# Kernel tuning notes

Hardware: AMD Instinct MI355X
Metric: run time of the kernel (lower is better)

## Reference

```python
import jax, jax.numpy as jnp
import numpy as np

B, S, D = 4, 4096, 1024
H, HID, ATT = 16, 64, 64


def setup_inputs() -> dict:
    key = jax.random.key(0)
    ks = jax.random.split(key, 7)
    sc = 0.02
    return {
        "x": jax.random.normal(ks[0], (B, S, D), dtype=jnp.float32),
        "Wq": jax.random.normal(ks[1], (D, H * HID), dtype=jnp.float32) * sc,
        "bq": jnp.zeros((H * HID,), dtype=jnp.float32),
        "Wk": jax.random.normal(ks[2], (D, H * HID), dtype=jnp.float32) * sc,
        "bk": jnp.zeros((H * HID,), dtype=jnp.float32),
        "Wv": jax.random.normal(ks[3], (D, H * ATT), dtype=jnp.float32) * sc,
        "bv": jnp.zeros((H * ATT,), dtype=jnp.float32),
    }


def reference(x, Wq, bq, Wk, bk, Wv, bv):
    b, s, _ = x.shape
    q = (x @ Wq + bq).reshape(b, s, H, HID)
    k = (x @ Wk + bk).reshape(b, s, H, HID)
    v = (x @ Wv + bv).reshape(b, s, H, ATT)
    # attention across the head axis: [B,S,H,H] scores per token
    scores = jnp.einsum("bsid,bsjd->bsij", q, k) / np.sqrt(HID).astype(np.float32)
    probs = jax.nn.softmax(scores, axis=-1)
    ctx = jnp.einsum("bsij,bsja->bsia", probs, v)
    return ctx.reshape(b, s, H * ATT)
```

## Files before the change

kernel.cpp:

```cpp
#include <hip/hip_runtime.h>


#define AS1 __attribute__((address_space(1)))
#define AS3 __attribute__((address_space(3)))

typedef __bf16 bf16x8 __attribute__((ext_vector_type(8)));
typedef float f32x4 __attribute__((ext_vector_type(4)));
typedef unsigned short u16x8 __attribute__((ext_vector_type(8)));

static constexpr int MTOK = 16384;
static constexpr int N3   = 3072;
static constexpr int KD   = 1024;

__device__ __forceinline__ unsigned short f2bf(float f) {
  unsigned u = __float_as_uint(f);
  unsigned r = u + 0x7FFFu + ((u >> 16) & 1u);
  return (unsigned short)(r >> 16);
}
__device__ __forceinline__ float bf2f(unsigned short s) {
  return __uint_as_float(((unsigned)s) << 16);
}

__device__ __forceinline__ void gload_lds16(const void* g, void* lds_uniform) {
  __builtin_amdgcn_global_load_lds((const AS1 void*)g, (AS3 void*)lds_uniform, 16, 0, 0);
}

__global__ __launch_bounds__(256) void cvt_x_kernel(const float* __restrict__ x,
                                                    unsigned short* __restrict__ xb) {
  int i = blockIdx.x * 256 + threadIdx.x;
  const float4* p = (const float4*)x;
  float4 a = p[2 * i], b = p[2 * i + 1];
  u16x8 o;
  o[0] = f2bf(a.x); o[1] = f2bf(a.y); o[2] = f2bf(a.z); o[3] = f2bf(a.w);
  o[4] = f2bf(b.x); o[5] = f2bf(b.y); o[6] = f2bf(b.z); o[7] = f2bf(b.w);
  *((u16x8*)xb + i) = o;
}

__global__ __launch_bounds__(256) void prep_w_kernel(const float* __restrict__ Wq,
                                                     const float* __restrict__ Wk,
                                                     const float* __restrict__ Wv,
                                                     const float* __restrict__ bq,
                                                     const float* __restrict__ bk,
                                                     const float* __restrict__ bv,
                                                     unsigned short* __restrict__ WT,
                                                     float* __restrict__ bcat) {
  __shared__ float tile[32][33];
  int kt = blockIdx.x * 32;
  int nt = blockIdx.y * 32;
  const float* W; const float* bias; int nb;
  if (nt < 1024)      { W = Wq; bias = bq; nb = nt; }
  else if (nt < 2048) { W = Wk; bias = bk; nb = nt - 1024; }
  else                { W = Wv; bias = bv; nb = nt - 2048; }
  int tx = threadIdx.x & 31, ty = threadIdx.x >> 5;
#pragma unroll
  for (int it = 0; it < 4; ++it) {
    int kk = it * 8 + ty;
    tile[kk][tx] = W[(size_t)(kt + kk) * 1024 + nb + tx];
  }
  __syncthreads();
#pragma unroll
  for (int it = 0; it < 4; ++it) {
    int nn = it * 8 + ty;
    WT[(size_t)(nt + nn) * 1024 + kt + tx] = f2bf(tile[tx][nn]);
  }
  if (blockIdx.x == 0 && threadIdx.x < 32)
    bcat[nt + threadIdx.x] = bias[nb + threadIdx.x];
}

__global__ __launch_bounds__(512, 2) void gemm_qkv_kernel(const unsigned short* __restrict__ A,
                                                          const unsigned short* __restrict__ Bt,
                                                          const float* __restrict__ bias,
                                                          unsigned short* __restrict__ C) {
  __shared__ __align__(16) unsigned short lds[65536];
  const int tid  = threadIdx.x;
  const int lane = tid & 63;
  const int wave = tid >> 6;
  const int wm = wave >> 2, wn = wave & 3;
  const int m0 = blockIdx.x * 256;
  const int n0 = blockIdx.y * 256;
  const int chunk = lane >> 4;
  const int hl = lane & 15;

  const int srow = tid >> 2;
  const int sc   = ((tid & 3) ^ ((srow >> 1) & 3)) * 8;
  const size_t asrc0 = (size_t)(m0 + srow) * KD + sc;
  const size_t asrc1 = (size_t)(m0 + 128 + srow) * KD + sc;
  const size_t bsrc0 = (size_t)(n0 + srow) * KD + sc;
  const size_t bsrc1 = (size_t)(n0 + 128 + srow) * KD + sc;

  int aoff[8], boff[4];
#pragma unroll
  for (int m = 0; m < 8; ++m) {
    int row = wm * 128 + m * 16 + hl;
    aoff[m] = row * 32 + (chunk ^ ((row >> 1) & 3)) * 8;
  }
#pragma unroll
  for (int n = 0; n < 4; ++n) {
    int row = wn * 64 + n * 16 + hl;
    boff[n] = 8192 + row * 32 + (chunk ^ ((row >> 1) & 3)) * 8;
  }

  f32x4 acc[8][4] = {};

#define STAGE(SLOT, KK)                                                        \
  do {                                                                         \
    unsigned short* dst = lds + (SLOT) * 16384 + tid * 8;                      \
    gload_lds16(A  + asrc0 + (KK), dst);                                       \
    gload_lds16(A  + asrc1 + (KK), dst + 4096);                                \
    gload_lds16(Bt + bsrc0 + (KK), dst + 8192);                                \
    gload_lds16(Bt + bsrc1 + (KK), dst + 12288);                               \
  } while (0)

#define PH(SLOT, DOSTAGE, STSLOT, KREAD)                                       \
  do {                                                                         \
    const unsigned short* bufp = lds + (SLOT) * 16384;                         \
    bf16x8 af[8], bfr[4];                                                      \
    _Pragma("unroll") for (int m = 0; m < 8; ++m)                              \
      af[m] = *(const bf16x8*)(bufp + aoff[m]);                                \
    _Pragma("unroll") for (int n = 0; n < 4; ++n)                              \
      bfr[n] = *(const bf16x8*)(bufp + boff[n]);                               \
    if (DOSTAGE) { STAGE(STSLOT, (KREAD) + 96); }                              \
    __builtin_amdgcn_s_barrier();                             \
    asm volatile("s_waitcnt lgkmcnt(0)" ::: "memory");                         \
    __builtin_amdgcn_sched_barrier(0);                                         \
    __builtin_amdgcn_s_setprio(1);                                             \
    _Pragma("unroll") for (int m = 0; m < 8; ++m)                              \
      _Pragma("unroll") for (int n = 0; n < 4; ++n)                            \
        acc[m][n] = __builtin_amdgcn_mfma_f32_16x16x32_bf16(af[m], bfr[n],     \
                                                            acc[m][n], 0, 0, 0);\
    __builtin_amdgcn_s_setprio(0);                                             \
  } while (0)

#define SYNC(VM)                                                               \
  do {                                                                         \
    asm volatile("s_waitcnt vmcnt(" #VM ")" ::: "memory");                     \
    __builtin_amdgcn_s_barrier();                             \
    __builtin_amdgcn_sched_barrier(0);                                         \
  } while (0)

  STAGE(0, 0); STAGE(1, 32); STAGE(2, 64);

#pragma unroll 1
  for (int t = 0; t < 7; ++t) {
    const int kb = t * 128;
    SYNC(8); PH(0, true, 3, kb);
    SYNC(8); PH(1, true, 0, kb + 32);
    SYNC(8); PH(2, true, 1, kb + 64);
    SYNC(8); PH(3, true, 2, kb + 96);
  }
  SYNC(8); PH(0, true, 3, 896);
  SYNC(8); PH(1, false, 0, 928);
  SYNC(4); PH(2, false, 0, 960);
  SYNC(0); PH(3, false, 0, 992);
#undef STAGE
#undef PH
#undef SYNC

#pragma unroll
  for (int n = 0; n < 4; ++n) {
    int col = n0 + wn * 64 + n * 16 + hl;
    float bvv = bias[col];
#pragma unroll
    for (int m = 0; m < 8; ++m) {
      int rowb = m0 + wm * 128 + m * 16 + chunk * 4;
#pragma unroll
      for (int r = 0; r < 4; ++r) {
        C[(size_t)(rowb + r) * N3 + col] = f2bf(acc[m][n][r] + bvv);
      }
    }
  }
}

__global__ __launch_bounds__(256) void attn_kernel(const unsigned short* __restrict__ qkv,
                                                   float* __restrict__ out) {
  __shared__ float p_lds[4][16][17];
  const int tid = threadIdx.x;
  const int lane = tid & 63;
  const int w = tid >> 6;
  const size_t token = (size_t)blockIdx.x * 4 + w;
  const unsigned short* rowp = qkv + token * N3;
  const int head = lane & 15;
  const int chunk = lane >> 4;

  const int o = head * 64 + chunk * 8;
  bf16x8 q0 = *(const bf16x8*)(rowp + o);
  bf16x8 q1 = *(const bf16x8*)(rowp + o + 32);
  bf16x8 k0 = *(const bf16x8*)(rowp + 1024 + o);
  bf16x8 k1 = *(const bf16x8*)(rowp + 1024 + o + 32);
  f32x4 c = {0.f, 0.f, 0.f, 0.f};
  c = __builtin_amdgcn_mfma_f32_16x16x32_bf16(q0, k0, c, 0, 0, 0);
  c = __builtin_amdgcn_mfma_f32_16x16x32_bf16(q1, k1, c, 0, 0, 0);

#pragma unroll
  for (int r = 0; r < 4; ++r) {
    float s = c[r] * 0.125f;
    float m = s;
#pragma unroll
    for (int off = 1; off < 16; off <<= 1) m = fmaxf(m, __shfl_xor(m, off, 64));
    float e = __expf(s - m);
    float sum = e;
#pragma unroll
    for (int off = 1; off < 16; off <<= 1) sum += __shfl_xor(sum, off, 64);
    p_lds[w][chunk * 4 + r][head] = e / sum;
  }
  __syncthreads();

  const int i = lane >> 2;
  const int ab = lane & 3;
  const unsigned short* vbase = rowp + 2048 + ab * 16;
  float accv[16];
#pragma unroll
  for (int cc = 0; cc < 16; ++cc) accv[cc] = 0.f;
#pragma unroll
  for (int j = 0; j < 16; ++j) {
    float pij = p_lds[w][i][j];
    u16x8 v0 = *(const u16x8*)(vbase + j * 64);
    u16x8 v1 = *(const u16x8*)(vbase + j * 64 + 8);
#pragma unroll
    for (int cc = 0; cc < 8; ++cc) accv[cc] += pij * bf2f(v0[cc]);
#pragma unroll
    for (int cc = 0; cc < 8; ++cc) accv[8 + cc] += pij * bf2f(v1[cc]);
  }
  float* op = out + token * 1024 + i * 64 + ab * 16;
#pragma unroll
  for (int cc = 0; cc < 16; cc += 4) {
    f32x4 v = {accv[cc], accv[cc + 1], accv[cc + 2], accv[cc + 3]};
    *(f32x4*)(op + cc) = v;
  }
}

extern "C" void kernel_launch(void* const* d_in, const int* in_sizes, int n_in,
                              void* d_out, int out_size, void* d_ws, size_t ws_size,
                              hipStream_t stream) {
  const float* x  = (const float*)d_in[0];
  const float* Wq = (const float*)d_in[1];
  const float* bq = (const float*)d_in[2];
  const float* Wk = (const float*)d_in[3];
  const float* bk = (const float*)d_in[4];
  const float* Wv = (const float*)d_in[5];
  const float* bv = (const float*)d_in[6];
  float* out = (float*)d_out;

  char* ws = (char*)d_ws;
  unsigned short* xb   = (unsigned short*)ws;
  unsigned short* WT   = (unsigned short*)(ws + 33554432);
  float*          bcat = (float*)(ws + 39845888);
  unsigned short* qkv  = (unsigned short*)(ws + 39858176);

  cvt_x_kernel<<<dim3((MTOK * KD / 8) / 256), 256, 0, stream>>>(x, xb);
  prep_w_kernel<<<dim3(32, 96), 256, 0, stream>>>(Wq, Wk, Wv, bq, bk, bv, WT, bcat);
  gemm_qkv_kernel<<<dim3(MTOK / 256, N3 / 256), 512, 0, stream>>>(xb, WT, bcat, qkv);
  attn_kernel<<<dim3(MTOK / 4), 256, 0, stream>>>(qkv, out);
}
```

Baseline: 175.3 us.

## Split each GEMM k-slice into two half-phases interleaving loads with MFMAs

Each 32-wide k-slice of the QKV projection GEMM now runs as two half-phases, each computing half of the M fragments. The A-tile global-to-LDS loads are issued in the first half and the B-tile loads in the second, so LDS reads and prefetch traffic are spread across the MFMA work. This adds an extra barrier per slice, keeps A register pressure at half the fragments, and moves the vmcnt wait to the end of each slice.

```diff
diff --git a/kernel.cpp b/kernel.cpp
--- a/kernel.cpp
+++ b/kernel.cpp
@@ -102,7 +102,7 @@
 
   f32x4 acc[8][4] = {};
 
-#define STAGE(SLOT, KK)                                                        \
+#define STAGE4(SLOT, KK)                                                       \
   do {                                                                         \
     unsigned short* dst = lds + (SLOT) * 16384 + tid * 8;                      \
     gload_lds16(A  + asrc0 + (KK), dst);                                       \
@@ -111,50 +111,71 @@
     gload_lds16(Bt + bsrc1 + (KK), dst + 12288);                               \
   } while (0)
 
-#define PH(SLOT, DOSTAGE, STSLOT, KREAD)                                       \
+#define SLICE(SLOT, DOSTAGE, KSTG, VM)                                         \
   do {                                                                         \
     const unsigned short* bufp = lds + (SLOT) * 16384;                         \
-    bf16x8 af[8], bfr[4];                                                      \
-    _Pragma("unroll") for (int m = 0; m < 8; ++m)                              \
-      af[m] = *(const bf16x8*)(bufp + aoff[m]);                                \
+    unsigned short* dst = lds + (((SLOT) + 3) & 3) * 16384 + tid * 8;          \
+    bf16x8 a0[4], a1[4], bb[4];                                                \
+           \
     _Pragma("unroll") for (int n = 0; n < 4; ++n)                              \
-      bfr[n] = *(const bf16x8*)(bufp + boff[n]);                               \
-    if (DOSTAGE) { STAGE(STSLOT, (KREAD) + 96); }                              \
-    __builtin_amdgcn_s_barrier();                             \
+      bb[n] = *(const bf16x8*)(bufp + boff[n]);                                \
+    _Pragma("unroll") for (int m = 0; m < 4; ++m)                              \
+      a0[m] = *(const bf16x8*)(bufp + aoff[m]);                                \
+    if (DOSTAGE) {                                                             \
+      gload_lds16(A + asrc0 + (KSTG), dst);                                    \
+      gload_lds16(A + asrc1 + (KSTG), dst + 4096);                             \
+    }                                                                          \
+    __builtin_amdgcn_s_barrier();                                              \
     asm volatile("s_waitcnt lgkmcnt(0)" ::: "memory");                         \
     __builtin_amdgcn_sched_barrier(0);                                         \
     __builtin_amdgcn_s_setprio(1);                                             \
-    _Pragma("unroll") for (int m = 0; m < 8; ++m)                              \
+    _Pragma("unroll") for (int m = 0; m < 4; ++m)                              \
       _Pragma("unroll") for (int n = 0; n < 4; ++n)                            \
-        acc[m][n] = __builtin_amdgcn_mfma_f32_16x16x32_bf16(af[m], bfr[n],     \
+        acc[m][n] = __builtin_amdgcn_mfma_f32_16x16x32_bf16(a0[m], bb[n],      \
                                                             acc[m][n], 0, 0, 0);\
     __builtin_amdgcn_s_setprio(0);                                             \
+    __builtin_amdgcn_s_barrier();                                              \
+    __builtin_amdgcn_sched_barrier(0);                                         \
+                 \
+    _Pragma("unroll") for (int m = 0; m < 4; ++m)                              \
+      a1[m] = *(const bf16x8*)(bufp + aoff[4 + m]);                            \
+    if (DOSTAGE) {                                                             \
+      gload_lds16(Bt + bsrc0 + (KSTG), dst + 8192);                            \
+      gload_lds16(Bt + bsrc1 + (KSTG), dst + 12288);                           \
+    }                                                                          \
+    __builtin_amdgcn_s_barrier();                                              \
+    asm volatile("s_waitcnt lgkmcnt(0)" ::: "memory");                         \
+    __builtin_amdgcn_sched_barrier(0);                                         \
+    __builtin_amdgcn_s_setprio(1);                                             \
+    _Pragma("unroll") for (int m = 0; m < 4; ++m)                              \
+      _Pragma("unroll") for (int n = 0; n < 4; ++n)                            \
+        acc[4 + m][n] = __builtin_amdgcn_mfma_f32_16x16x32_bf16(a1[m], bb[n],  \
+                                                        acc[4 + m][n], 0, 0, 0);\
+    __builtin_amdgcn_s_setprio(0);                                             \
+    asm volatile("s_waitcnt vmcnt(" #VM ")" ::: "memory");                     \
+    __builtin_amdgcn_s_barrier();                                              \
+    __builtin_amdgcn_sched_barrier(0);                                         \
   } while (0)
 
-#define SYNC(VM)                                                               \
-  do {                                                                         \
-    asm volatile("s_waitcnt vmcnt(" #VM ")" ::: "memory");                     \
-    __builtin_amdgcn_s_barrier();                             \
-    __builtin_amdgcn_sched_barrier(0);                                         \
-  } while (0)
-
-  STAGE(0, 0); STAGE(1, 32); STAGE(2, 64);
+  STAGE4(0, 0); STAGE4(1, 32); STAGE4(2, 64);
+  asm volatile("s_waitcnt vmcnt(8)" ::: "memory");
+  __builtin_amdgcn_s_barrier();
+  __builtin_amdgcn_sched_barrier(0);
 
 #pragma unroll 1
   for (int t = 0; t < 7; ++t) {
     const int kb = t * 128;
-    SYNC(8); PH(0, true, 3, kb);
-    SYNC(8); PH(1, true, 0, kb + 32);
-    SYNC(8); PH(2, true, 1, kb + 64);
-    SYNC(8); PH(3, true, 2, kb + 96);
-  }
-  SYNC(8); PH(0, true, 3, 896);
-  SYNC(8); PH(1, false, 0, 928);
-  SYNC(4); PH(2, false, 0, 960);
-  SYNC(0); PH(3, false, 0, 992);
-#undef STAGE
-#undef PH
-#undef SYNC
+    SLICE(0, true, kb + 96, 8);
+    SLICE(1, true, kb + 128, 8);
+    SLICE(2, true, kb + 160, 8);
+    SLICE(3, true, kb + 192, 8);
+  }
+  SLICE(0, true, 992, 8);
+  SLICE(1, false, 0, 4);
+  SLICE(2, false, 0, 0);
+  SLICE(3, false, 0, 0);
+#undef STAGE4
+#undef SLICE
 
 #pragma unroll
   for (int n = 0; n < 4; ++n) {
```

Result: no change. 175.5 us (+0.1%).
